# Kernel tuning notes

Hardware: AMD Instinct MI355X
Metric: run time of the kernel (lower is better)

## Reference

```python
import jax, jax.numpy as jnp
import numpy as np

D, H, KVH, HD = 2048, 16, 8, 128
D1, D2 = 32, 64  # get_decompose_dim(2048)
BITS = 8


def fake_quant(x, bits=BITS):
    # per-row (last-axis) symmetric fake quant with straight-through estimator
    qmax = float(2 ** (bits - 1) - 1)
    s = jnp.maximum(jnp.max(jnp.abs(x), axis=-1, keepdims=True) / qmax, 1e-8)
    q = jnp.clip(jnp.round(x / s), -qmax, qmax) * s
    return x + jax.lax.stop_gradient(q - x)


def rotate_half(x):
    h = x.shape[-1] // 2
    return jnp.concatenate([-x[..., h:], x[..., :h]], axis=-1)


def setup_inputs() -> dict:
    key = jax.random.key(0)
    ks = jax.random.split(key, 10)
    B, S = 1, 2048
    hidden_states = jax.random.normal(ks[0], (B, S, D), jnp.float32)
    # rotary embeddings
    inv_freq = 1.0 / (10000.0 ** (jnp.arange(0, HD, 2, dtype=jnp.float32) / HD))
    t = jnp.arange(S, dtype=jnp.float32)
    freqs = t[:, None] * inv_freq[None, :]
    emb = jnp.concatenate([freqs, freqs], axis=-1)
    cos, sin = jnp.cos(emb)[None], jnp.sin(emb)[None]  # [1,S,HD]
    # projection weights
    Wq = jax.random.normal(ks[1], (H * HD, D), jnp.float32) * 0.02
    Wk = jax.random.normal(ks[2], (KVH * HD, D), jnp.float32) * 0.02
    Wv = jax.random.normal(ks[3], (KVH * HD, D), jnp.float32) * 0.02
    Wo = jax.random.normal(ks[4], (D, H * HD), jnp.float32) * 0.02
    # learned invertible transforms (near-identity for conditioning)
    L = jnp.eye(D1) + 0.02 * jax.random.normal(ks[5], (D1, D1), jnp.float32)
    R = jnp.eye(D2) + 0.02 * jax.random.normal(ks[6], (D2, D2), jnp.float32)
    diag = 1.0 + 0.1 * jax.random.uniform(ks[7], (D,), jnp.float32)
    Tk = jnp.eye(HD) + 0.02 * jax.random.normal(ks[8], (HD, HD), jnp.float32)
    Tv = jnp.eye(HD) + 0.02 * jax.random.normal(ks[9], (HD, HD), jnp.float32)
    return dict(hidden_states=hidden_states, cos=cos, sin=sin, Wq=Wq, Wk=Wk,
                Wv=Wv, Wo=Wo, L=L, R=R, diag=diag, Tk=Tk, Tv=Tv)


def reference(hidden_states, cos, sin, Wq, Wk, Wv, Wo, L, R, diag, Tk, Tv):
    B, S, _ = hidden_states.shape
    groups = H // KVH
    scale = HD ** -0.5
    # ---- ln_trans: x' = (x * diag) @ kron(L, R) ----
    P = diag[:, None] * jnp.kron(L, R)               # [D, D]
    Pinv = jnp.kron(jnp.linalg.inv(L), jnp.linalg.inv(R)) * (1.0 / diag)[None, :]
    x = hidden_states @ P
    x_q = fake_quant(x)                               # per-token activation quant
    # ---- QKV with transform fused into weights (qa_trans), then weight quant ----
    q = x_q @ fake_quant(Wq @ Pinv.T).T               # [B,S,H*HD]
    k = x_q @ fake_quant(Wk @ Pinv.T).T               # [B,S,KVH*HD]
    Wv_eff = jnp.einsum('hd,khD->kdD', Tv, (Wv @ Pinv.T).reshape(KVH, HD, D))
    v = x_q @ fake_quant(Wv_eff.reshape(KVH * HD, D)).T  # v already in Tv space
    # ---- heads + RoPE ----
    q = q.reshape(B, S, H, HD).transpose(0, 2, 1, 3)
    k = k.reshape(B, S, KVH, HD).transpose(0, 2, 1, 3)
    v = v.reshape(B, S, KVH, HD).transpose(0, 2, 1, 3)
    c, s_ = cos[:, None], sin[:, None]                # [1,1,S,HD]
    q = q * c + rotate_half(q) * s_
    k = k * c + rotate_half(k) * s_
    # ---- kcache trans + quant: q @ inv(Tk)^T, k @ Tk (dot product preserved) ----
    q = q @ jnp.linalg.inv(Tk).T
    k = fake_quant(k @ Tk)
    v = fake_quant(v)
    # ---- eager causal attention with GQA ----
    k = jnp.repeat(k, groups, axis=1)
    v = jnp.repeat(v, groups, axis=1)
    scores = jnp.einsum('bhqd,bhkd->bhqk', q, k) * scale
    mask = jnp.tril(jnp.ones((S, S), bool))
    scores = jnp.where(mask, scores, jnp.finfo(scores.dtype).min)
    w = jax.nn.softmax(scores, axis=-1)
    o = jnp.einsum('bhqk,bhkd->bhqd', w, v)
    o = o.transpose(0, 2, 1, 3).reshape(B, S, H * HD)
    # ---- undo vcache trans per head, then quantized o_proj ----
    o = (o.reshape(B, S, H, HD) @ jnp.linalg.inv(Tv)).reshape(B, S, H * HD)
    out = fake_quant(o) @ fake_quant(Wo).T
    return out
```

## Files before the change

### kernel.cpp

```cpp
#include <hip/hip_runtime.h>
#include <math.h>

typedef unsigned short u16;
typedef __attribute__((ext_vector_type(8))) short bf16x8;
typedef __attribute__((ext_vector_type(4))) float f32x4;

__device__ __forceinline__ u16 f2bf(float x) {
    union { float f; unsigned int u; } c; c.f = x;
    unsigned int r = c.u + 0x7fffu + ((c.u >> 16) & 1u);
    return (u16)(r >> 16);
}
__device__ __forceinline__ float bf2f(u16 h) {
    union { unsigned int u; float f; } c; c.u = ((unsigned int)h) << 16;
    return c.f;
}
__device__ __forceinline__ bf16x8 ld16(const u16* p) {
    bf16x8 r;
    ((uint2*)&r)[0] = *(const uint2*)p;
    ((uint2*)&r)[1] = *(const uint2*)(p + 4);
    return r;
}
__device__ __forceinline__ void st8(u16* dst, uint4 r) {
    *(uint2*)dst = make_uint2(r.x, r.y);
    *(uint2*)(dst + 4) = make_uint2(r.z, r.w);
}

__global__ __launch_bounds__(1024) void gj4_kernel(
    const float* __restrict__ A0, float* __restrict__ I0,
    const float* __restrict__ A1, float* __restrict__ I1,
    const float* __restrict__ A2, float* __restrict__ I2,
    const float* __restrict__ A3, float* __restrict__ I3) {
    __shared__ float rowbuf[2][128];
    const float* A; float* out; int N;
    switch (blockIdx.x) {
        case 0:  A = A0; out = I0; N = 32;  break;
        case 1:  A = A1; out = I1; N = 64;  break;
        case 2:  A = A2; out = I2; N = 128; break;
        default: A = A3; out = I3; N = 128; break;
    }
    const int tid = threadIdx.x;
    const int i = tid >> 3, g = tid & 7, c0 = g * 16;
    const int rl = (i & 7) << 3;
    float r[16];
#pragma unroll
    for (int e = 0; e < 16; ++e) {
        int j = c0 + e;
        r[e] = (i < N && j < N) ? A[i * N + j] : ((i == j) ? 1.0f : 0.0f);
    }
    if (i == 0) {
        float ip = 1.0f / __shfl(r[0], rl, 64);
#pragma unroll
        for (int e = 0; e < 16; ++e)
            rowbuf[0][c0 + e] = (c0 + e == 0) ? ip : r[e] * ip;
    }
    __syncthreads();
    const int ng = N >> 4;
    for (int k16 = 0; k16 < ng; ++k16) {
#pragma unroll
        for (int e = 0; e < 16; ++e) {
            const int k = (k16 << 4) + e;
            const int pb = k & 1;
            float ci = __shfl(r[e], rl + k16, 64);
            float4 rb0 = *(const float4*)&rowbuf[pb][c0];
            float4 rb1 = *(const float4*)&rowbuf[pb][c0 + 4];
            float4 rb2 = *(const float4*)&rowbuf[pb][c0 + 8];
            float4 rb3 = *(const float4*)&rowbuf[pb][c0 + 12];
            float rb[16] = {rb0.x, rb0.y, rb0.z, rb0.w, rb1.x, rb1.y, rb1.z, rb1.w,
                            rb2.x, rb2.y, rb2.z, rb2.w, rb3.x, rb3.y, rb3.z, rb3.w};
            if (i == k) {
#pragma unroll
                for (int e2 = 0; e2 < 16; ++e2) r[e2] = rb[e2];
            } else {
#pragma unroll
                for (int e2 = 0; e2 < 16; ++e2) {
                    float v = (c0 + e2 == k) ? 0.0f : r[e2];
                    r[e2] = fmaf(-ci, rb[e2], v);
                }
            }
            if (k + 1 < N && i == k + 1) {
                const int en = (e + 1) & 15;
                const int gn = (e == 15) ? k16 + 1 : k16;
                float ip = 1.0f / __shfl(r[en], rl + gn, 64);
#pragma unroll
                for (int e2 = 0; e2 < 16; ++e2)
                    rowbuf[pb ^ 1][c0 + e2] = (c0 + e2 == k + 1) ? ip : r[e2] * ip;
            }
            __syncthreads();
        }
    }
    if (i < N)
#pragma unroll
        for (int e = 0; e < 16; ++e) {
            int j = c0 + e;
            if (j < N) out[i * N + j] = r[e];
        }
}

__global__ void rdiag_kernel(const float* __restrict__ d, float* __restrict__ rd) {
    int i = blockIdx.x * 256 + threadIdx.x;
    rd[i] = 1.0f / d[i];
}

template <int TA, int TB, int OUTQ>
__global__ __launch_bounds__(256) void kron_kernel(
    const float* __restrict__ X, const float* __restrict__ scIn,
    const float* __restrict__ A, const float* __restrict__ B,
    u16* __restrict__ Yq, float* __restrict__ Ysc, float* __restrict__ Yf) {
    __shared__ float Al[32 * 33];
    __shared__ float Bl[64 * 65];
    __shared__ float Xl[32 * 65];
    __shared__ float Tl[32 * 65];
    __shared__ float red[256];
    const int tid = threadIdx.x;
    for (int idx = tid; idx < 1024; idx += 256) {
        int c = idx >> 5, a = idx & 31;
        Al[c * 33 + a] = TA ? A[a * 32 + c] : A[c * 32 + a];
    }
    for (int idx = tid; idx < 4096; idx += 256) {
        int d = idx >> 6, b = idx & 63;
        Bl[d * 65 + b] = TB ? B[b * 64 + d] : B[d * 64 + b];
    }
    const int row = blockIdx.x;
    const float* xp = X + (size_t)row * 2048;
    for (int j = tid; j < 2048; j += 256)
        Xl[(j >> 6) * 65 + (j & 63)] = xp[j] * scIn[j];
    __syncthreads();

    const int c = tid >> 3, b0 = (tid & 7) * 8;
    float t[8];
#pragma unroll
    for (int jj = 0; jj < 8; ++jj) t[jj] = 0.0f;
    for (int d = 0; d < 64; ++d) {
        float xv = Xl[c * 65 + d];
#pragma unroll
        for (int jj = 0; jj < 8; ++jj)
            t[jj] = fmaf(xv, Bl[d * 65 + b0 + jj], t[jj]);
    }
#pragma unroll
    for (int jj = 0; jj < 8; ++jj) Tl[c * 65 + b0 + jj] = t[jj];
    __syncthreads();

    const int a = tid >> 3;
    float y[8];
#pragma unroll
    for (int jj = 0; jj < 8; ++jj) y[jj] = 0.0f;
    for (int c2 = 0; c2 < 32; ++c2) {
        float av = Al[c2 * 33 + a];
#pragma unroll
        for (int jj = 0; jj < 8; ++jj)
            y[jj] = fmaf(av, Tl[c2 * 65 + b0 + jj], y[jj]);
    }

    if (OUTQ) {
        float am = 0.0f;
#pragma unroll
        for (int jj = 0; jj < 8; ++jj) am = fmaxf(am, fabsf(y[jj]));
        red[tid] = am;
        __syncthreads();
        for (int s = 128; s > 0; s >>= 1) {
            if (tid < s) red[tid] = fmaxf(red[tid], red[tid + s]);
            __syncthreads();
        }
        float scale = fmaxf(red[0] / 127.0f, 1e-8f);
        if (tid == 0) Ysc[row] = scale;
        u16 qq[8];
#pragma unroll
        for (int e = 0; e < 8; ++e) {
            float v = rintf(y[e] / scale);
            v = fminf(fmaxf(v, -127.0f), 127.0f);
            qq[e] = f2bf(v);
        }
        uint4 pk;
        pk.x = qq[0] | ((unsigned)qq[1] << 16); pk.y = qq[2] | ((unsigned)qq[3] << 16);
        pk.z = qq[4] | ((unsigned)qq[5] << 16); pk.w = qq[6] | ((unsigned)qq[7] << 16);
        *(uint4*)(Yq + (size_t)row * 2048 + tid * 8) = pk;
    } else {
        float* yp = Yf + (size_t)row * 2048 + tid * 8;
        *(float4*)yp = make_float4(y[0], y[1], y[2], y[3]);
        *(float4*)(yp + 4) = make_float4(y[4], y[5], y[6], y[7]);
    }
}

__global__ void split_s_kernel(const float* __restrict__ in, int ld, int cols,
                               u16* __restrict__ hi, u16* __restrict__ lo) {
    int idx = (blockIdx.x * 256 + threadIdx.x) * 4;
    int r = idx / cols, c = idx % cols;
    float4 v = *(const float4*)(in + (size_t)r * ld + c);
    ushort4 h, l;
    h.x = f2bf(v.x); l.x = f2bf(v.x - bf2f(h.x));
    h.y = f2bf(v.y); l.y = f2bf(v.y - bf2f(h.y));
    h.z = f2bf(v.z); l.z = f2bf(v.z - bf2f(h.z));
    h.w = f2bf(v.w); l.w = f2bf(v.w - bf2f(h.w));
    *(ushort4*)(hi + idx) = h;
    *(ushort4*)(lo + idx) = l;
}

__global__ void split_t_kernel(const float* __restrict__ in, u16* __restrict__ hi,
                               u16* __restrict__ lo, int rows, int cols) {
    __shared__ float t[32][33];
    int bx = blockIdx.x, by = blockIdx.y;
    int lx = threadIdx.x & 31, ly = threadIdx.x >> 5;
    for (int r = ly; r < 32; r += 8)
        t[r][lx] = in[(size_t)(by * 32 + r) * cols + bx * 32 + lx];
    __syncthreads();
    for (int r = ly; r < 32; r += 8) {
        float v = t[lx][r];
        size_t o = (size_t)(bx * 32 + r) * rows + by * 32 + lx;
        u16 h = f2bf(v);
        hi[o] = h;
        lo[o] = f2bf(v - bf2f(h));
    }
}

__global__ void trans16_kernel(const u16* __restrict__ in, u16* __restrict__ out,
                               int rows, int cols) {
    __shared__ u16 t[64][72];
    int bx = blockIdx.x, by = blockIdx.y;
    int tid = threadIdx.x;
#pragma unroll
    for (int it = 0; it < 2; ++it) {
        int ii = tid + it * 256;
        int r = ii >> 3, c8 = (ii & 7) * 8;
        uint4 v = *(const uint4*)(in + (size_t)(by * 64 + r) * cols + bx * 64 + c8);
        st8(&t[r][c8], v);
    }
    __syncthreads();
#pragma unroll
    for (int it = 0; it < 2; ++it) {
        int ii = tid + it * 256;
        int r = ii >> 3, c8 = (ii & 7) * 8;
        u16 tmp[8];
#pragma unroll
        for (int e = 0; e < 8; ++e) tmp[e] = t[c8 + e][r];
        uint4 v;
        v.x = tmp[0] | ((unsigned)tmp[1] << 16); v.y = tmp[2] | ((unsigned)tmp[3] << 16);
        v.z = tmp[4] | ((unsigned)tmp[5] << 16); v.w = tmp[6] | ((unsigned)tmp[7] << 16);
        *(uint4*)(out + (size_t)(bx * 64 + r) * rows + by * 64 + c8) = v;
    }
}

__global__ __launch_bounds__(256) void gemm_kernel(
    const u16* __restrict__ Ah, const u16* __restrict__ Al, int lda, long aZ, int aDiv,
    const u16* __restrict__ Bh, const u16* __restrict__ Bl, int ldb, long bZ, int bDiv,
    float* __restrict__ C, int ldc, long cZ, int cDiv, int K, float alpha) {
    const int m0 = blockIdx.y * 128, n0 = blockIdx.x * 128;
    const int z = blockIdx.z;
    {
        long ao = (long)(z >> aDiv) * aZ;
        long bo = (long)(z >> bDiv) * bZ;
        Ah += ao; Al += ao; Bh += bo; Bl += bo;
    }
    __shared__ u16 Ash[2][2][128][36];
    __shared__ u16 Bsh[2][2][128][36];

    const int tid = threadIdx.x, lane = tid & 63, wave = tid >> 6;
    const int wr = wave >> 1, wc = wave & 1;
    const int fr = lane & 15, fg8 = (lane >> 4) * 8;
    const int srow = tid >> 2, cc8 = (tid & 3) * 8;

    f32x4 acc[4][4];
#pragma unroll
    for (int m = 0; m < 4; ++m)
#pragma unroll
        for (int n = 0; n < 4; ++n) acc[m][n] = (f32x4)0.0f;

    uint4 rah0, rah1, ral0, ral1, rbh0, rbh1, rbl0, rbl1;
    const size_t aoff0 = (size_t)(m0 + srow) * lda + cc8;
    const size_t aoff1 = aoff0 + (size_t)64 * lda;
    const size_t boff0 = (size_t)(n0 + srow) * ldb + cc8;
    const size_t boff1 = boff0 + (size_t)64 * ldb;

#define G_LOAD(k0) { \
    rah0 = *(const uint4*)(Ah + aoff0 + (k0)); rah1 = *(const uint4*)(Ah + aoff1 + (k0)); \
    ral0 = *(const uint4*)(Al + aoff0 + (k0)); ral1 = *(const uint4*)(Al + aoff1 + (k0)); \
    rbh0 = *(const uint4*)(Bh + boff0 + (k0)); rbh1 = *(const uint4*)(Bh + boff1 + (k0)); \
    rbl0 = *(const uint4*)(Bl + boff0 + (k0)); rbl1 = *(const uint4*)(Bl + boff1 + (k0)); }
#define G_STORE(b) { \
    st8(&Ash[b][0][srow][cc8], rah0); st8(&Ash[b][0][srow + 64][cc8], rah1); \
    st8(&Ash[b][1][srow][cc8], ral0); st8(&Ash[b][1][srow + 64][cc8], ral1); \
    st8(&Bsh[b][0][srow][cc8], rbh0); st8(&Bsh[b][0][srow + 64][cc8], rbh1); \
    st8(&Bsh[b][1][srow][cc8], rbl0); st8(&Bsh[b][1][srow + 64][cc8], rbl1); }

    const int nk = K >> 5;
    G_LOAD(0);
    G_STORE(0);
    __syncthreads();
    int cur = 0;
    for (int ik = 0; ik < nk; ++ik) {
        if (ik + 1 < nk) G_LOAD((ik + 1) << 5);
        bf16x8 bh[4], bl[4];
#pragma unroll
        for (int n = 0; n < 4; ++n) {
            bh[n] = ld16(&Bsh[cur][0][wc * 64 + n * 16 + fr][fg8]);
            bl[n] = ld16(&Bsh[cur][1][wc * 64 + n * 16 + fr][fg8]);
        }
#pragma unroll
        for (int m = 0; m < 4; ++m) {
            bf16x8 ah = ld16(&Ash[cur][0][wr * 64 + m * 16 + fr][fg8]);
            bf16x8 al = ld16(&Ash[cur][1][wr * 64 + m * 16 + fr][fg8]);
#pragma unroll
            for (int n = 0; n < 4; ++n) {
                acc[m][n] = __builtin_amdgcn_mfma_f32_16x16x32_bf16(ah, bh[n], acc[m][n], 0, 0, 0);
                acc[m][n] = __builtin_amdgcn_mfma_f32_16x16x32_bf16(ah, bl[n], acc[m][n], 0, 0, 0);
                acc[m][n] = __builtin_amdgcn_mfma_f32_16x16x32_bf16(al, bh[n], acc[m][n], 0, 0, 0);
            }
        }
        if (ik + 1 < nk) G_STORE(cur ^ 1);
        __syncthreads();
        cur ^= 1;
    }
    const long co = (long)(z >> cDiv) * cZ;
#pragma unroll
    for (int m = 0; m < 4; ++m) {
        int row_b = m0 + wr * 64 + m * 16 + (fg8 >> 1);
#pragma unroll
        for (int n = 0; n < 4; ++n) {
            int col = n0 + wc * 64 + n * 16 + fr;
#pragma unroll
            for (int j = 0; j < 4; ++j)
                C[co + (long)(row_b + j) * ldc + col] = alpha * acc[m][n][j];
        }
    }
#undef G_LOAD
#undef G_STORE
}

__global__ __launch_bounds__(256) void gemm_int_kernel(
    const u16* __restrict__ A, int lda, const float* __restrict__ sa,
    const u16* __restrict__ B, int ldb, const float* __restrict__ sb,
    float* __restrict__ C, int ldc, long aZ, long bZ, long cZ, int K) {
    const int m0 = blockIdx.y * 128, n0 = blockIdx.x * 128;
    const int z = blockIdx.z;
    A += (long)z * aZ; B += (long)z * bZ; C += (long)z * cZ;
    __shared__ u16 Ash[2][128][36];
    __shared__ u16 Bsh[2][128][36];
    const int tid = threadIdx.x, lane = tid & 63, wave = tid >> 6;
    const int wr = wave >> 1, wc = wave & 1;
    const int fr = lane & 15, fg8 = (lane >> 4) * 8;
    const int srow = tid >> 2, cc8 = (tid & 3) * 8;
    f32x4 acc[4][4];
#pragma unroll
    for (int m = 0; m < 4; ++m)
#pragma unroll
        for (int n = 0; n < 4; ++n) acc[m][n] = (f32x4)0.0f;

    uint4 ra0, ra1, rb0, rb1;
    const size_t aoff0 = (size_t)(m0 + srow) * lda + cc8;
    const size_t aoff1 = aoff0 + (size_t)64 * lda;
    const size_t boff0 = (size_t)(n0 + srow) * ldb + cc8;
    const size_t boff1 = boff0 + (size_t)64 * ldb;
#define GI_LOAD(k0) { \
    ra0 = *(const uint4*)(A + aoff0 + (k0)); ra1 = *(const uint4*)(A + aoff1 + (k0)); \
    rb0 = *(const uint4*)(B + boff0 + (k0)); rb1 = *(const uint4*)(B + boff1 + (k0)); }
#define GI_STORE(b) { \
    st8(&Ash[b][srow][cc8], ra0); st8(&Ash[b][srow + 64][cc8], ra1); \
    st8(&Bsh[b][srow][cc8], rb0); st8(&Bsh[b][srow + 64][cc8], rb1); }
    const int nk = K >> 5;
    GI_LOAD(0);
    GI_STORE(0);
    __syncthreads();
    int cur = 0;
    for (int ik = 0; ik < nk; ++ik) {
        if (ik + 1 < nk) GI_LOAD((ik + 1) << 5);
        bf16x8 bfr[4];
#pragma unroll
        for (int n = 0; n < 4; ++n)
            bfr[n] = ld16(&Bsh[cur][wc * 64 + n * 16 + fr][fg8]);
#pragma unroll
        for (int m = 0; m < 4; ++m) {
            bf16x8 ah = ld16(&Ash[cur][wr * 64 + m * 16 + fr][fg8]);
#pragma unroll
            for (int n = 0; n < 4; ++n)
                acc[m][n] = __builtin_amdgcn_mfma_f32_16x16x32_bf16(ah, bfr[n], acc[m][n], 0, 0, 0);
        }
        if (ik + 1 < nk) GI_STORE(cur ^ 1);
        __syncthreads();
        cur ^= 1;
    }
#pragma unroll
    for (int m = 0; m < 4; ++m) {
        int row_b = m0 + wr * 64 + m * 16 + (fg8 >> 1);
#pragma unroll
        for (int n = 0; n < 4; ++n) {
            int col = n0 + wc * 64 + n * 16 + fr;
            float sc = sb[col];
#pragma unroll
            for (int j = 0; j < 4; ++j)
                C[(long)(row_b + j) * ldc + col] = acc[m][n][j] * sa[row_b + j] * sc;
        }
    }
#undef GI_LOAD
#undef GI_STORE
}

__global__ void rowquant_int_kernel(const float* __restrict__ x, u16* __restrict__ qi,
                                    float* __restrict__ sc, int cols) {
    __shared__ float red[256];
    int row = blockIdx.x, tid = threadIdx.x;
    const float* p = x + (size_t)row * cols;
    u16* q = qi + (size_t)row * cols;
    float m = 0.0f;
    for (int j = tid; j < cols; j += 256) m = fmaxf(m, fabsf(p[j]));
    red[tid] = m; __syncthreads();
    for (int s = 128; s > 0; s >>= 1) {
        if (tid < s) red[tid] = fmaxf(red[tid], red[tid + s]);
        __syncthreads();
    }
    float scale = fmaxf(red[0] / 127.0f, 1e-8f);
    if (tid == 0) sc[row] = scale;
    for (int j = tid; j < cols; j += 256) {
        float v = rintf(p[j] / scale);
        v = fminf(fmaxf(v, -127.0f), 127.0f);
        q[j] = f2bf(v);
    }
}

__global__ void rowquant_v_kernel(const float* __restrict__ x, int ld, int cb,
                                  u16* __restrict__ qi, float* __restrict__ sc) {
    int row = blockIdx.x;
    int lane = threadIdx.x & 63, w = threadIdx.x >> 6;
    if (w > 0) return;
    const float* p = x + (size_t)(row >> 3) * ld + cb + (row & 7) * 128;
    u16* q = qi + (size_t)row * 128;
    float2 v = *(const float2*)(p + lane * 2);
    float m = fmaxf(fabsf(v.x), fabsf(v.y));
#pragma unroll
    for (int off = 1; off < 64; off <<= 1) m = fmaxf(m, __shfl_xor(m, off));
    float scale = fmaxf(m / 127.0f, 1e-8f);
    if (lane == 0) sc[row] = scale;
    float a = rintf(v.x / scale), b = rintf(v.y / scale);
    a = fminf(fmaxf(a, -127.0f), 127.0f);
    b = fminf(fmaxf(b, -127.0f), 127.0f);
    unsigned pk = f2bf(a) | ((unsigned)f2bf(b) << 16);
    *(unsigned*)(q + lane * 2) = pk;
}

__global__ void rope_kernel(float* __restrict__ x, int ld, int cb,
                            const float* __restrict__ c, const float* __restrict__ s,
                            int nh) {
    int idx = blockIdx.x * 256 + threadIdx.x;
    int d = idx & 63;
    int t = idx >> 6;
    int h = t % nh;
    int sq = t / nh;
    size_t base = (size_t)sq * ld + cb + h * 128;
    float a = x[base + d], b = x[base + d + 64];
    float c1 = c[sq * 128 + d], s1 = s[sq * 128 + d];
    float c2 = c[sq * 128 + d + 64], s2 = s[sq * 128 + d + 64];
    x[base + d] = a * c1 - b * s1;
    x[base + d + 64] = b * c2 + a * s2;
}

__global__ __launch_bounds__(256, 2) void flash_kernel(
    const float* __restrict__ q2f,
    const u16* __restrict__ k2i, const float* __restrict__ ksc,
    const u16* __restrict__ vTi, const float* __restrict__ vsc,
    float* __restrict__ obuf, float* __restrict__ mlbuf) {
    const int h = blockIdx.x, part = blockIdx.y, qt = 31 - blockIdx.z, g = h >> 1;
    __shared__ u16 Ksh[2][64 * 128];
    __shared__ u16 Vsh[2][128 * 64];
    __shared__ u16 Psh[4][16 * 64];
    __shared__ float Kss[2][64];
    __shared__ float Vss[2][64];

    const int tid = threadIdx.x, lane = tid & 63, w = tid >> 6;
    const int lc = lane & 15, lg = lane >> 4;
    const float scale = 0.08838834764831845f;
    const float LOG2E = 1.4426950408889634f;
    const float THR = 10.0f;

    bf16x8 qh[4], ql[4];
    {
        int s = qt * 64 + w * 16 + lc;
        const float* qp = q2f + (size_t)s * 2048 + h * 128 + lg * 8;
#pragma unroll
        for (int kk = 0; kk < 4; ++kk) {
            float4 v0 = *(const float4*)(qp + kk * 32);
            float4 v1 = *(const float4*)(qp + kk * 32 + 4);
            float vv[8] = {v0.x, v0.y, v0.z, v0.w, v1.x, v1.y, v1.z, v1.w};
#pragma unroll
            for (int e = 0; e < 8; ++e) {
                float x = vv[e] * scale;
                u16 hh = f2bf(x);
                qh[kk][e] = (short)hh;
                ql[kk][e] = (short)f2bf(x - bf2f(hh));
            }
        }
    }

    f32x4 acc_o[8];
#pragma unroll
    for (int nn = 0; nn < 8; ++nn) acc_o[nn] = (f32x4)0.0f;
    float mj = -1e30f, lj = 0.0f;

    const int p0cnt = (qt + 2) >> 1;
    const int tn = (part == 0) ? p0cnt : (qt + 1 - p0cnt);
    const int t0 = (part == 0) ? 0 : p0cnt;

    const int kr = tid >> 2, kc = tid & 3;
    const int vd = tid >> 1, vc0 = (tid & 1) * 4;
    uint4 kg0, kg1, kg2, kg3, vg0, vg1, vg2, vg3;
    float sreg = 0.0f;

#define STAGE_LOAD(tg) { \
    const int j0_ = (tg) * 64; \
    const u16* kp_ = k2i + (size_t)(j0_ + kr) * 1024 + g * 128; \
    kg0 = *(const uint4*)(kp_ + kc * 8); \
    kg1 = *(const uint4*)(kp_ + (kc + 4) * 8); \
    kg2 = *(const uint4*)(kp_ + (kc + 8) * 8); \
    kg3 = *(const uint4*)(kp_ + (kc + 12) * 8); \
    const u16* vp_ = vTi + (size_t)(g * 128 + vd) * 2048 + j0_; \
    vg0 = *(const uint4*)(vp_ + vc0 * 8); \
    vg1 = *(const uint4*)(vp_ + (vc0 + 1) * 8); \
    vg2 = *(const uint4*)(vp_ + (vc0 + 2) * 8); \
    vg3 = *(const uint4*)(vp_ + (vc0 + 3) * 8); \
    if (tid < 64) sreg = ksc[(j0_ + tid) * 8 + g] * LOG2E; \
    else if (tid < 128) sreg = vsc[(j0_ + tid - 64) * 8 + g]; }

#define STAGE_WRITE(b) { \
    *(uint4*)(&Ksh[b][kr * 128 + ((kc ^ (kr & 7)) << 3)]) = kg0; \
    *(uint4*)(&Ksh[b][kr * 128 + (((kc + 4) ^ (kr & 7)) << 3)]) = kg1; \
    *(uint4*)(&Ksh[b][kr * 128 + (((kc + 8) ^ (kr & 7)) << 3)]) = kg2; \
    *(uint4*)(&Ksh[b][kr * 128 + (((kc + 12) ^ (kr & 7)) << 3)]) = kg3; \
    *(uint4*)(&Vsh[b][vd * 64 + ((vc0 ^ (vd & 7)) << 3)]) = vg0; \
    *(uint4*)(&Vsh[b][vd * 64 + (((vc0 + 1) ^ (vd & 7)) << 3)]) = vg1; \
    *(uint4*)(&Vsh[b][vd * 64 + (((vc0 + 2) ^ (vd & 7)) << 3)]) = vg2; \
    *(uint4*)(&Vsh[b][vd * 64 + (((vc0 + 3) ^ (vd & 7)) << 3)]) = vg3; \
    if (tid < 64) Kss[b][tid] = sreg; \
    else if (tid < 128) Vss[b][tid - 64] = sreg; }

    if (tn > 0) {
        STAGE_LOAD(t0);
        STAGE_WRITE(0);
    }
    __syncthreads();
    for (int t = 0; t < tn; ++t) {
        const int cur = t & 1;
        const int tg = t0 + t;
        if (t + 1 < tn) STAGE_LOAD(t0 + t + 1);

        f32x4 accs[4];
#pragma unroll
        for (int n = 0; n < 4; ++n) accs[n] = (f32x4)0.0f;
#pragma unroll
        for (int n = 0; n < 4; ++n) {
#pragma unroll
            for (int kk = 0; kk < 4; ++kk) {
                bf16x8 kf = ld16(&Ksh[cur][(n * 16 + lc) * 128 + (((kk * 4 + lg) ^ (lc & 7)) << 3)]);
                accs[n] = __builtin_amdgcn_mfma_f32_16x16x32_bf16(kf, qh[kk], accs[n], 0, 0, 0);
                accs[n] = __builtin_amdgcn_mfma_f32_16x16x32_bf16(kf, ql[kk], accs[n], 0, 0, 0);
            }
        }
#pragma unroll
        for (int n = 0; n < 4; ++n)
#pragma unroll
            for (int j = 0; j < 4; ++j)
                accs[n][j] *= Kss[cur][n * 16 + lg * 4 + j];
        if (tg == qt) {
            int qg = qt * 64 + w * 16 + lc;
#pragma unroll
            for (int n = 0; n < 4; ++n)
#pragma unroll
                for (int j = 0; j < 4; ++j) {
                    int kgl = tg * 64 + n * 16 + lg * 4 + j;
                    if (kgl > qg) accs[n][j] = -3.0e38f;
                }
        }

        float pm = accs[0][0];
#pragma unroll
        for (int n = 0; n < 4; ++n)
#pragma unroll
            for (int j = 0; j < 4; ++j) pm = fmaxf(pm, accs[n][j]);
        pm = fmaxf(pm, __shfl_xor(pm, 16));
        pm = fmaxf(pm, __shfl_xor(pm, 32));
        bool need = pm > mj + THR;
        float mn = need ? pm : mj;
        float sf = need ? exp2f(mj - mn) : 1.0f;
        mj = mn;
        if (__any(need)) {
            float sfj[4];
#pragma unroll
            for (int j = 0; j < 4; ++j) sfj[j] = __shfl(sf, lg * 4 + j);
#pragma unroll
            for (int nn = 0; nn < 8; ++nn)
#pragma unroll
                for (int j = 0; j < 4; ++j) acc_o[nn][j] *= sfj[j];
        }
        float rowsum = 0.0f;
#pragma unroll
        for (int n = 0; n < 4; ++n)
#pragma unroll
            for (int j = 0; j < 4; ++j) {
                float p = exp2f(accs[n][j] - mj);
                accs[n][j] = p;
                rowsum += p;
            }
        rowsum += __shfl_xor(rowsum, 16);
        rowsum += __shfl_xor(rowsum, 32);
        lj = lj * sf + rowsum;

#pragma unroll
        for (int n = 0; n < 4; ++n)
#pragma unroll
            for (int jp = 0; jp < 2; ++jp) {
                int k = n * 16 + lg * 4 + jp * 2;
                unsigned val = f2bf(accs[n][jp * 2] * Vss[cur][k]) |
                               ((unsigned)f2bf(accs[n][jp * 2 + 1] * Vss[cur][k + 1]) << 16);
                int cch = k >> 3;
                *(unsigned*)(&Psh[w][lc * 64 + ((cch ^ (lc & 7)) << 3) + (k & 7)]) = val;
            }
        bf16x8 pf[2];
#pragma unroll
        for (int kk = 0; kk < 2; ++kk)
            pf[kk] = ld16(&Psh[w][lc * 64 + (((kk * 4 + lg) ^ (lc & 7)) << 3)]);

#pragma unroll
        for (int nn = 0; nn < 8; ++nn) {
            int d = nn * 16 + lc;
#pragma unroll
            for (int kk = 0; kk < 2; ++kk) {
                bf16x8 vf = ld16(&Vsh[cur][d * 64 + (((kk * 4 + lg) ^ (d & 7)) << 3)]);
                acc_o[nn] = __builtin_amdgcn_mfma_f32_16x16x32_bf16(pf[kk], vf, acc_o[nn], 0, 0, 0);
            }
        }
        if (t + 1 < tn) STAGE_WRITE(cur ^ 1);
        __syncthreads();
    }
#undef STAGE_LOAD
#undef STAGE_WRITE

    float* op = obuf + (size_t)part * 4194304 + ((size_t)h * 2048 + qt * 64 + w * 16) * 128;
#pragma unroll
    for (int nn = 0; nn < 8; ++nn)
#pragma unroll
        for (int j = 0; j < 4; ++j)
            op[(lg * 4 + j) * 128 + nn * 16 + lc] = acc_o[nn][j];
    if (lg == 0) {
        int rs = h * 2048 + qt * 64 + w * 16 + lc;
        mlbuf[part * 65536 + rs] = mj;
        mlbuf[part * 65536 + 32768 + rs] = lj;
    }
}

__global__ void combine_split_kernel(const float* __restrict__ o01,
                                     const float* __restrict__ ml,
                                     u16* __restrict__ oh, u16* __restrict__ ol) {
    int idx = blockIdx.x * 256 + threadIdx.x;
    int hs = idx >> 7;
    float m0 = ml[hs], l0 = ml[32768 + hs];
    float m1 = ml[65536 + hs], l1 = ml[98304 + hs];
    float m = fmaxf(m0, m1);
    float w0 = exp2f(m0 - m), w1 = exp2f(m1 - m);
    float l = l0 * w0 + l1 * w1;
    float v = (o01[idx] * w0 + o01[4194304 + idx] * w1) / l;
    u16 h = f2bf(v);
    oh[idx] = h;
    ol[idx] = f2bf(v - bf2f(h));
}

__global__ void add2_kernel(const float* __restrict__ a, const float* __restrict__ b,
                            float* __restrict__ o) {
    int i = (blockIdx.x * 256 + threadIdx.x) * 4;
    float4 x = *(const float4*)(a + i);
    float4 y = *(const float4*)(b + i);
    x.x += y.x; x.y += y.y; x.z += y.z; x.w += y.w;
    *(float4*)(o + i) = x;
}

extern "C" void kernel_launch(void* const* d_in, const int* in_sizes, int n_in,
                              void* d_out, int out_size, void* d_ws, size_t ws_size,
                              hipStream_t stream) {
    const float* hidden = (const float*)d_in[0];
    const float* cosp   = (const float*)d_in[1];
    const float* sinp   = (const float*)d_in[2];
    const float* Wq     = (const float*)d_in[3];
    const float* Wk     = (const float*)d_in[4];
    const float* Wv     = (const float*)d_in[5];
    const float* Wo     = (const float*)d_in[6];
    const float* Lp     = (const float*)d_in[7];
    const float* Rp     = (const float*)d_in[8];
    const float* diag   = (const float*)d_in[9];
    const float* Tkp    = (const float*)d_in[10];
    const float* Tvp    = (const float*)d_in[11];
    float* out = (float*)d_out;

    const size_t MiB = 1ull << 20;
    char* W = (char*)d_ws;
    auto F = [&](size_t mb) { return (float*)(W + mb * MiB); };
    auto U = [&](size_t mb) { return (u16*)(W + mb * MiB); };
    const long HP2 = 2097152;

    float* dsc   = (float*)d_out;
    float* invL  = dsc;
    float* invR  = dsc + 1024;
    float* invTk = dsc + 5120;
    float* invTv = dsc + 21504;
    u16* sm = (u16*)(dsc + 37888);
    u16* invTk_sh = sm;              u16* invTk_sl = sm + 16384;
    u16* TkT_sh   = sm + 2 * 16384;  u16* TkT_sl   = sm + 3 * 16384;
    u16* invTvT_sh= sm + 4 * 16384;  u16* invTvT_sl= sm + 5 * 16384;
    u16* TvT_sh   = sm + 6 * 16384;  u16* TvT_sl   = sm + 7 * 16384;

    auto gemm = [&](dim3 grid,
                    const u16* Ah, const u16* Al, int lda, long aZ, int aDiv,
                    const u16* Bh, const u16* Bl, int ldb, long bZ, int bDiv,
                    float* C, int ldc, long cZ, int cDiv, int K, float alpha) {
        gemm_kernel<<<grid, 256, 0, stream>>>(Ah, Al, lda, aZ, aDiv,
            Bh, Bl, ldb, bZ, bDiv, C, ldc, cZ, cDiv, K, alpha);
    };

    float* xs    = F(88);
    float* wqkvs = xs + 2048;
    float* wqs   = wqkvs;
    float* wks   = wqkvs + 2048;
    float* wvs   = wqkvs + 3072;
    float* k2s   = wqkvs + 4096;
    float* vs    = k2s + 16384;
    float* o2s   = vs + 16384;
    float* wos   = o2s + 2048;
    float* rdiag = wos + 2048;

    gj4_kernel<<<4, 1024, 0, stream>>>(Lp, invL, Rp, invR, Tkp, invTk, Tvp, invTv);
    rdiag_kernel<<<8, 256, 0, stream>>>(diag, rdiag);
    split_s_kernel<<<16, 256, 0, stream>>>(invTk, 128, 128, invTk_sh, invTk_sl);
    split_t_kernel<<<dim3(4, 4), 256, 0, stream>>>(Tkp, TkT_sh, TkT_sl, 128, 128);
    split_t_kernel<<<dim3(4, 4), 256, 0, stream>>>(invTv, invTvT_sh, invTvT_sl, 128, 128);
    split_t_kernel<<<dim3(4, 4), 256, 0, stream>>>(Tvp, TvT_sh, TvT_sl, 128, 128);

    u16* Xi    = U(0);
    u16* WQKVi = U(8);
    u16* WVi   = U(20);
    float* WvP = F(24);
    kron_kernel<0, 0, 1><<<2048, 256, 0, stream>>>(hidden, diag, Lp, Rp, Xi, xs, 0);
    kron_kernel<1, 1, 1><<<2048, 256, 0, stream>>>(Wq, rdiag, invL, invR, WQKVi, wqs, 0);
    kron_kernel<1, 1, 1><<<1024, 256, 0, stream>>>(Wk, rdiag, invL, invR, U(16), wks, 0);
    kron_kernel<1, 1, 0><<<1024, 256, 0, stream>>>(Wv, rdiag, invL, invR, 0, 0, WvP);

    u16* WVPt_s = U(32);
    split_t_kernel<<<dim3(64, 32), 256, 0, stream>>>(WvP, WVPt_s, WVPt_s + HP2, 1024, 2048);
    float* WVf = F(72);
    gemm(dim3(16, 1, 8), TvT_sh, TvT_sl, 128, 0, 0,
         WVPt_s, WVPt_s + HP2, 1024, 128, 0, WVf, 2048, (long)128 * 2048, 0, 128, 1.0f);
    rowquant_int_kernel<<<1024, 256, 0, stream>>>(WVf, WVi, wvs, 2048);

    float* QKVf = F(40);
    gemm_int_kernel<<<dim3(32, 16), 256, 0, stream>>>(Xi, 2048, xs, WQKVi, 2048, wqkvs,
                                                      QKVf, 4096, 0, 0, 0, 2048);

    rope_kernel<<<8192, 256, 0, stream>>>(QKVf, 4096, 0, cosp, sinp, 16);
    rope_kernel<<<4096, 256, 0, stream>>>(QKVf, 4096, 2048, cosp, sinp, 8);

    u16* KB_s = U(24);
    split_s_kernel<<<2048, 256, 0, stream>>>(QKVf + 2048, 4096, 1024, KB_s, KB_s + HP2);
    float* k2f = F(32);
    gemm(dim3(1, 16, 8), KB_s, KB_s + HP2, 1024, 128, 0,
         TkT_sh, TkT_sl, 128, 0, 0, k2f, 1024, 128, 0, 128, 1.0f);
    u16* k2i = U(8);
    rowquant_int_kernel<<<16384, 256, 0, stream>>>(k2f, k2i, k2s, 128);

    u16* Vi = U(12);
    rowquant_v_kernel<<<16384, 64, 0, stream>>>(QKVf, 4096, 3072, Vi, vs);
    u16* vTi = U(16);
    trans16_kernel<<<dim3(16, 32), 256, 0, stream>>>(Vi, vTi, 2048, 1024);

    u16* Q_s = U(24);
    split_s_kernel<<<4096, 256, 0, stream>>>(QKVf, 4096, 2048, Q_s, Q_s + 4194304);
    float* q2f = F(72);
    gemm(dim3(1, 16, 16), Q_s, Q_s + 4194304, 2048, 128, 0,
         invTk_sh, invTk_sl, 128, 0, 0, q2f, 2048, 128, 0, 128, 1.0f);

    float* o01 = F(40);
    float* ml  = F(32);
    flash_kernel<<<dim3(16, 2, 32), 256, 0, stream>>>(q2f, k2i, k2s, vTi, vs, o01, ml);
    u16* o_s = U(0);
    combine_split_kernel<<<16384, 256, 0, stream>>>(o01, ml, o_s, o_s + 4194304);

    float* o2f = F(16);
    gemm(dim3(1, 16, 16), o_s, o_s + 4194304, 128, 262144, 0,
         invTvT_sh, invTvT_sl, 128, 0, 0, o2f, 2048, 128, 0, 128, 1.0f);
    u16* o2i = U(32);
    rowquant_int_kernel<<<2048, 256, 0, stream>>>(o2f, o2i, o2s, 2048);
    u16* Woi = U(40);
    rowquant_int_kernel<<<2048, 256, 0, stream>>>(Wo, Woi, wos, 2048);
    float* C0 = F(48);
    gemm_int_kernel<<<dim3(16, 16, 2), 256, 0, stream>>>(o2i, 2048, o2s, Woi, 2048, wos,
                                                         C0, 2048, 1024, 1024, 4194304, 1024);
    add2_kernel<<<4096, 256, 0, stream>>>(C0, C0 + 4194304, out);

    (void)in_sizes; (void)n_in; (void)out_size; (void)ws_size;
}
```

Baseline: 511.0 us.

## Fuse fp32-to-bf16 split into GEMM loads and merge small prep kernels

```diff
diff --git a/kernel.cpp b/kernel.cpp
--- a/kernel.cpp
+++ b/kernel.cpp
@@ -23,6 +23,20 @@
 __device__ __forceinline__ void st8(u16* dst, uint4 r) {
     *(uint2*)dst = make_uint2(r.x, r.y);
     *(uint2*)(dst + 4) = make_uint2(r.z, r.w);
+}
+__device__ __forceinline__ void cvt8(const float4& v0, const float4& v1,
+                                     uint4& hi, uint4& lo) {
+    float vv[8] = {v0.x, v0.y, v0.z, v0.w, v1.x, v1.y, v1.z, v1.w};
+    u16 h[8], l[8];
+#pragma unroll
+    for (int e = 0; e < 8; ++e) {
+        h[e] = f2bf(vv[e]);
+        l[e] = f2bf(vv[e] - bf2f(h[e]));
+    }
+    hi.x = h[0] | ((unsigned)h[1] << 16); hi.y = h[2] | ((unsigned)h[3] << 16);
+    hi.z = h[4] | ((unsigned)h[5] << 16); hi.w = h[6] | ((unsigned)h[7] << 16);
+    lo.x = l[0] | ((unsigned)l[1] << 16); lo.y = l[2] | ((unsigned)l[3] << 16);
+    lo.z = l[4] | ((unsigned)l[5] << 16); lo.w = l[6] | ((unsigned)l[7] << 16);
 }
 
 __global__ __launch_bounds__(1024) void gj4_kernel(
@@ -96,12 +110,7 @@
         }
 }
 
-__global__ void rdiag_kernel(const float* __restrict__ d, float* __restrict__ rd) {
-    int i = blockIdx.x * 256 + threadIdx.x;
-    rd[i] = 1.0f / d[i];
-}
-
-template <int TA, int TB, int OUTQ>
+template <int TA, int TB, int OUTQ, int DIV>
 __global__ __launch_bounds__(256) void kron_kernel(
     const float* __restrict__ X, const float* __restrict__ scIn,
     const float* __restrict__ A, const float* __restrict__ B,
@@ -122,8 +131,10 @@
     }
     const int row = blockIdx.x;
     const float* xp = X + (size_t)row * 2048;
-    for (int j = tid; j < 2048; j += 256)
-        Xl[(j >> 6) * 65 + (j & 63)] = xp[j] * scIn[j];
+    for (int j = tid; j < 2048; j += 256) {
+        float sc = DIV ? (1.0f / scIn[j]) : scIn[j];
+        Xl[(j >> 6) * 65 + (j & 63)] = xp[j] * sc;
+    }
     __syncthreads();
 
     const int c = tid >> 3, b0 = (tid & 7) * 8;
@@ -212,30 +223,30 @@
     }
 }
 
-__global__ void trans16_kernel(const u16* __restrict__ in, u16* __restrict__ out,
-                               int rows, int cols) {
-    __shared__ u16 t[64][72];
+__global__ void split_t3_kernel(const float* __restrict__ i0, u16* __restrict__ h0,
+                                u16* __restrict__ l0,
+                                const float* __restrict__ i1, u16* __restrict__ h1,
+                                u16* __restrict__ l1,
+                                const float* __restrict__ i2, u16* __restrict__ h2,
+                                u16* __restrict__ l2) {
+    __shared__ float t[32][33];
+    const float* in; u16* hi; u16* lo;
+    switch (blockIdx.z) {
+        case 0:  in = i0; hi = h0; lo = l0; break;
+        case 1:  in = i1; hi = h1; lo = l1; break;
+        default: in = i2; hi = h2; lo = l2; break;
+    }
     int bx = blockIdx.x, by = blockIdx.y;
-    int tid = threadIdx.x;
-#pragma unroll
-    for (int it = 0; it < 2; ++it) {
-        int ii = tid + it * 256;
-        int r = ii >> 3, c8 = (ii & 7) * 8;
-        uint4 v = *(const uint4*)(in + (size_t)(by * 64 + r) * cols + bx * 64 + c8);
-        st8(&t[r][c8], v);
-    }
+    int lx = threadIdx.x & 31, ly = threadIdx.x >> 5;
+    for (int r = ly; r < 32; r += 8)
+        t[r][lx] = in[(size_t)(by * 32 + r) * 128 + bx * 32 + lx];
     __syncthreads();
-#pragma unroll
-    for (int it = 0; it < 2; ++it) {
-        int ii = tid + it * 256;
-        int r = ii >> 3, c8 = (ii & 7) * 8;
-        u16 tmp[8];
-#pragma unroll
-        for (int e = 0; e < 8; ++e) tmp[e] = t[c8 + e][r];
-        uint4 v;
-        v.x = tmp[0] | ((unsigned)tmp[1] << 16); v.y = tmp[2] | ((unsigned)tmp[3] << 16);
-        v.z = tmp[4] | ((unsigned)tmp[5] << 16); v.w = tmp[6] | ((unsigned)tmp[7] << 16);
-        *(uint4*)(out + (size_t)(bx * 64 + r) * rows + by * 64 + c8) = v;
+    for (int r = ly; r < 32; r += 8) {
+        float v = t[lx][r];
+        size_t o = (size_t)(bx * 32 + r) * 128 + by * 32 + lx;
+        u16 h = f2bf(v);
+        hi[o] = h;
+        lo[o] = f2bf(v - bf2f(h));
     }
 }
 
@@ -323,6 +334,95 @@
     }
 #undef G_LOAD
 #undef G_STORE
+}
+
+__global__ __launch_bounds__(256) void gemm_af32_kernel(
+    const float* __restrict__ A, int lda, long aZ, int aDiv,
+    const u16* __restrict__ Bh, const u16* __restrict__ Bl, int ldb, long bZ, int bDiv,
+    float* __restrict__ C, int ldc, long cZ, int cDiv, int K, float alpha) {
+    const int m0 = blockIdx.y * 128, n0 = blockIdx.x * 128;
+    const int z = blockIdx.z;
+    A += (long)(z >> aDiv) * aZ;
+    {
+        long bo = (long)(z >> bDiv) * bZ;
+        Bh += bo; Bl += bo;
+    }
+    __shared__ u16 Ash[2][2][128][36];
+    __shared__ u16 Bsh[2][2][128][36];
+
+    const int tid = threadIdx.x, lane = tid & 63, wave = tid >> 6;
+    const int wr = wave >> 1, wc = wave & 1;
+    const int fr = lane & 15, fg8 = (lane >> 4) * 8;
+    const int srow = tid >> 2, cc8 = (tid & 3) * 8;
+
+    f32x4 acc[4][4];
+#pragma unroll
+    for (int m = 0; m < 4; ++m)
+#pragma unroll
+        for (int n = 0; n < 4; ++n) acc[m][n] = (f32x4)0.0f;
+
+    float4 a00, a01, a10, a11;
+    uint4 rbh0, rbh1, rbl0, rbl1;
+    const size_t aoff0 = (size_t)(m0 + srow) * lda + cc8;
+    const size_t aoff1 = aoff0 + (size_t)64 * lda;
+    const size_t boff0 = (size_t)(n0 + srow) * ldb + cc8;
+    const size_t boff1 = boff0 + (size_t)64 * ldb;
+
+#define GA_LOAD(k0) { \
+    a00 = *(const float4*)(A + aoff0 + (k0)); a01 = *(const float4*)(A + aoff0 + (k0) + 4); \
+    a10 = *(const float4*)(A + aoff1 + (k0)); a11 = *(const float4*)(A + aoff1 + (k0) + 4); \
+    rbh0 = *(const uint4*)(Bh + boff0 + (k0)); rbh1 = *(const uint4*)(Bh + boff1 + (k0)); \
+    rbl0 = *(const uint4*)(Bl + boff0 + (k0)); rbl1 = *(const uint4*)(Bl + boff1 + (k0)); }
+#define GA_STORE(b) { \
+    uint4 h0_, l0_, h1_, l1_; \
+    cvt8(a00, a01, h0_, l0_); cvt8(a10, a11, h1_, l1_); \
+    st8(&Ash[b][0][srow][cc8], h0_); st8(&Ash[b][0][srow + 64][cc8], h1_); \
+    st8(&Ash[b][1][srow][cc8], l0_); st8(&Ash[b][1][srow + 64][cc8], l1_); \
+    st8(&Bsh[b][0][srow][cc8], rbh0); st8(&Bsh[b][0][srow + 64][cc8], rbh1); \
+    st8(&Bsh[b][1][srow][cc8], rbl0); st8(&Bsh[b][1][srow + 64][cc8], rbl1); }
+
+    const int nk = K >> 5;
+    GA_LOAD(0);
+    GA_STORE(0);
+    __syncthreads();
+    int cur = 0;
+    for (int ik = 0; ik < nk; ++ik) {
+        if (ik + 1 < nk) GA_LOAD((ik + 1) << 5);
+        bf16x8 bh[4], bl[4];
+#pragma unroll
+        for (int n = 0; n < 4; ++n) {
+            bh[n] = ld16(&Bsh[cur][0][wc * 64 + n * 16 + fr][fg8]);
+            bl[n] = ld16(&Bsh[cur][1][wc * 64 + n * 16 + fr][fg8]);
+        }
+#pragma unroll
+        for (int m = 0; m < 4; ++m) {
+            bf16x8 ah = ld16(&Ash[cur][0][wr * 64 + m * 16 + fr][fg8]);
+            bf16x8 al = ld16(&Ash[cur][1][wr * 64 + m * 16 + fr][fg8]);
+#pragma unroll
+            for (int n = 0; n < 4; ++n) {
+                acc[m][n] = __builtin_amdgcn_mfma_f32_16x16x32_bf16(ah, bh[n], acc[m][n], 0, 0, 0);
+                acc[m][n] = __builtin_amdgcn_mfma_f32_16x16x32_bf16(ah, bl[n], acc[m][n], 0, 0, 0);
+                acc[m][n] = __builtin_amdgcn_mfma_f32_16x16x32_bf16(al, bh[n], acc[m][n], 0, 0, 0);
+            }
+        }
+        if (ik + 1 < nk) GA_STORE(cur ^ 1);
+        __syncthreads();
+        cur ^= 1;
+    }
+    const long co = (long)(z >> cDiv) * cZ;
+#pragma unroll
+    for (int m = 0; m < 4; ++m) {
+        int row_b = m0 + wr * 64 + m * 16 + (fg8 >> 1);
+#pragma unroll
+        for (int n = 0; n < 4; ++n) {
+            int col = n0 + wc * 64 + n * 16 + fr;
+#pragma unroll
+            for (int j = 0; j < 4; ++j)
+                C[co + (long)(row_b + j) * ldc + col] = alpha * acc[m][n][j];
+        }
+    }
+#undef GA_LOAD
+#undef GA_STORE
 }
 
 __global__ __launch_bounds__(256) void gemm_int_kernel(
@@ -415,13 +515,11 @@
     }
 }
 
-__global__ void rowquant_v_kernel(const float* __restrict__ x, int ld, int cb,
-                                  u16* __restrict__ qi, float* __restrict__ sc) {
-    int row = blockIdx.x;
-    int lane = threadIdx.x & 63, w = threadIdx.x >> 6;
-    if (w > 0) return;
-    const float* p = x + (size_t)(row >> 3) * ld + cb + (row & 7) * 128;
-    u16* q = qi + (size_t)row * 128;
+__global__ void rowquant_w_kernel(const float* __restrict__ x, u16* __restrict__ qi,
+                                  float* __restrict__ sc) {
+    int row = blockIdx.x * 4 + (threadIdx.x >> 6);
+    int lane = threadIdx.x & 63;
+    const float* p = x + (size_t)row * 128;
     float2 v = *(const float2*)(p + lane * 2);
     float m = fmaxf(fabsf(v.x), fabsf(v.y));
 #pragma unroll
@@ -432,7 +530,52 @@
     a = fminf(fmaxf(a, -127.0f), 127.0f);
     b = fminf(fmaxf(b, -127.0f), 127.0f);
     unsigned pk = f2bf(a) | ((unsigned)f2bf(b) << 16);
-    *(unsigned*)(q + lane * 2) = pk;
+    *(unsigned*)(qi + (size_t)row * 128 + lane * 2) = pk;
+}
+
+__global__ __launch_bounds__(256) void quantT_v_kernel(
+    const float* __restrict__ QKVf, u16* __restrict__ vTi, float* __restrict__ vs) {
+    __shared__ u16 tile[128][72];
+    const int st = blockIdx.x, g = blockIdx.y;
+    const int t = threadIdx.x;
+    const int sl = t >> 2, dc = (t & 3) * 32;
+    const int s = st * 64 + sl;
+    const float* p = QKVf + (size_t)s * 4096 + 3072 + g * 128 + dc;
+    float4 vr[8];
+    float m = 0.0f;
+#pragma unroll
+    for (int q = 0; q < 8; ++q) {
+        vr[q] = *(const float4*)(p + q * 4);
+        m = fmaxf(m, fmaxf(fmaxf(fabsf(vr[q].x), fabsf(vr[q].y)),
+                           fmaxf(fabsf(vr[q].z), fabsf(vr[q].w))));
+    }
+    m = fmaxf(m, __shfl_xor(m, 1));
+    m = fmaxf(m, __shfl_xor(m, 2));
+    float scale = fmaxf(m / 127.0f, 1e-8f);
+    if ((t & 3) == 0) vs[s * 8 + g] = scale;
+#pragma unroll
+    for (int q = 0; q < 8; ++q) {
+        float vv[4] = {vr[q].x, vr[q].y, vr[q].z, vr[q].w};
+#pragma unroll
+        for (int e = 0; e < 4; ++e) {
+            float qv = rintf(vv[e] / scale);
+            qv = fminf(fmaxf(qv, -127.0f), 127.0f);
+            tile[dc + q * 4 + e][sl] = f2bf(qv);
+        }
+    }
+    __syncthreads();
+    const int d = t >> 1, sc0 = (t & 1) * 32;
+    u16* dst = vTi + (size_t)(g * 128 + d) * 2048 + st * 64 + sc0;
+#pragma unroll
+    for (int q = 0; q < 4; ++q) {
+        u16 tmp[8];
+#pragma unroll
+        for (int e = 0; e < 8; ++e) tmp[e] = tile[d][sc0 + q * 8 + e];
+        uint4 v;
+        v.x = tmp[0] | ((unsigned)tmp[1] << 16); v.y = tmp[2] | ((unsigned)tmp[3] << 16);
+        v.z = tmp[4] | ((unsigned)tmp[5] << 16); v.w = tmp[6] | ((unsigned)tmp[7] << 16);
+        *(uint4*)(dst + q * 8) = v;
+    }
 }
 
 __global__ void rope_kernel(float* __restrict__ x, int ld, int cb,
@@ -643,9 +786,9 @@
     }
 }
 
-__global__ void combine_split_kernel(const float* __restrict__ o01,
-                                     const float* __restrict__ ml,
-                                     u16* __restrict__ oh, u16* __restrict__ ol) {
+__global__ void combine_kernel(const float* __restrict__ o01,
+                               const float* __restrict__ ml,
+                               float* __restrict__ of) {
     int idx = blockIdx.x * 256 + threadIdx.x;
     int hs = idx >> 7;
     float m0 = ml[hs], l0 = ml[32768 + hs];
@@ -653,10 +796,7 @@
     float m = fmaxf(m0, m1);
     float w0 = exp2f(m0 - m), w1 = exp2f(m1 - m);
     float l = l0 * w0 + l1 * w1;
-    float v = (o01[idx] * w0 + o01[4194304 + idx] * w1) / l;
-    u16 h = f2bf(v);
-    oh[idx] = h;
-    ol[idx] = f2bf(v - bf2f(h));
+    of[idx] = (o01[idx] * w0 + o01[4194304 + idx] * w1) / l;
 }
 
 __global__ void add2_kernel(const float* __restrict__ a, const float* __restrict__ b,
@@ -702,14 +842,6 @@
     u16* invTvT_sh= sm + 4 * 16384;  u16* invTvT_sl= sm + 5 * 16384;
     u16* TvT_sh   = sm + 6 * 16384;  u16* TvT_sl   = sm + 7 * 16384;
 
-    auto gemm = [&](dim3 grid,
-                    const u16* Ah, const u16* Al, int lda, long aZ, int aDiv,
-                    const u16* Bh, const u16* Bl, int ldb, long bZ, int bDiv,
-                    float* C, int ldc, long cZ, int cDiv, int K, float alpha) {
-        gemm_kernel<<<grid, 256, 0, stream>>>(Ah, Al, lda, aZ, aDiv,
-            Bh, Bl, ldb, bZ, bDiv, C, ldc, cZ, cDiv, K, alpha);
-    };
-
     float* xs    = F(88);
     float* wqkvs = xs + 2048;
     float* wqs   = wqkvs;
@@ -719,29 +851,27 @@
     float* vs    = k2s + 16384;
     float* o2s   = vs + 16384;
     float* wos   = o2s + 2048;
-    float* rdiag = wos + 2048;
 
     gj4_kernel<<<4, 1024, 0, stream>>>(Lp, invL, Rp, invR, Tkp, invTk, Tvp, invTv);
-    rdiag_kernel<<<8, 256, 0, stream>>>(diag, rdiag);
     split_s_kernel<<<16, 256, 0, stream>>>(invTk, 128, 128, invTk_sh, invTk_sl);
-    split_t_kernel<<<dim3(4, 4), 256, 0, stream>>>(Tkp, TkT_sh, TkT_sl, 128, 128);
-    split_t_kernel<<<dim3(4, 4), 256, 0, stream>>>(invTv, invTvT_sh, invTvT_sl, 128, 128);
-    split_t_kernel<<<dim3(4, 4), 256, 0, stream>>>(Tvp, TvT_sh, TvT_sl, 128, 128);
+    split_t3_kernel<<<dim3(4, 4, 3), 256, 0, stream>>>(
+        Tkp, TkT_sh, TkT_sl, invTv, invTvT_sh, invTvT_sl, Tvp, TvT_sh, TvT_sl);
 
     u16* Xi    = U(0);
     u16* WQKVi = U(8);
     u16* WVi   = U(20);
     float* WvP = F(24);
-    kron_kernel<0, 0, 1><<<2048, 256, 0, stream>>>(hidden, diag, Lp, Rp, Xi, xs, 0);
-    kron_kernel<1, 1, 1><<<2048, 256, 0, stream>>>(Wq, rdiag, invL, invR, WQKVi, wqs, 0);
-    kron_kernel<1, 1, 1><<<1024, 256, 0, stream>>>(Wk, rdiag, invL, invR, U(16), wks, 0);
-    kron_kernel<1, 1, 0><<<1024, 256, 0, stream>>>(Wv, rdiag, invL, invR, 0, 0, WvP);
+    kron_kernel<0, 0, 1, 0><<<2048, 256, 0, stream>>>(hidden, diag, Lp, Rp, Xi, xs, 0);
+    kron_kernel<1, 1, 1, 1><<<2048, 256, 0, stream>>>(Wq, diag, invL, invR, WQKVi, wqs, 0);
+    kron_kernel<1, 1, 1, 1><<<1024, 256, 0, stream>>>(Wk, diag, invL, invR, U(16), wks, 0);
+    kron_kernel<1, 1, 0, 1><<<1024, 256, 0, stream>>>(Wv, diag, invL, invR, 0, 0, WvP);
 
     u16* WVPt_s = U(32);
     split_t_kernel<<<dim3(64, 32), 256, 0, stream>>>(WvP, WVPt_s, WVPt_s + HP2, 1024, 2048);
     float* WVf = F(72);
-    gemm(dim3(16, 1, 8), TvT_sh, TvT_sl, 128, 0, 0,
-         WVPt_s, WVPt_s + HP2, 1024, 128, 0, WVf, 2048, (long)128 * 2048, 0, 128, 1.0f);
+    gemm_kernel<<<dim3(16, 1, 8), 256, 0, stream>>>(
+        TvT_sh, TvT_sl, 128, 0, 0, WVPt_s, WVPt_s + HP2, 1024, 128, 0,
+        WVf, 2048, (long)128 * 2048, 0, 128, 1.0f);
     rowquant_int_kernel<<<1024, 256, 0, stream>>>(WVf, WVi, wvs, 2048);
 
     float* QKVf = F(40);
@@ -751,34 +881,31 @@
     rope_kernel<<<8192, 256, 0, stream>>>(QKVf, 4096, 0, cosp, sinp, 16);
     rope_kernel<<<4096, 256, 0, stream>>>(QKVf, 4096, 2048, cosp, sinp, 8);
 
-    u16* KB_s = U(24);
-    split_s_kernel<<<2048, 256, 0, stream>>>(QKVf + 2048, 4096, 1024, KB_s, KB_s + HP2);
     float* k2f = F(32);
-    gemm(dim3(1, 16, 8), KB_s, KB_s + HP2, 1024, 128, 0,
-         TkT_sh, TkT_sl, 128, 0, 0, k2f, 1024, 128, 0, 128, 1.0f);
+    gemm_af32_kernel<<<dim3(1, 16, 8), 256, 0, stream>>>(
+        QKVf + 2048, 4096, 128, 0, TkT_sh, TkT_sl, 128, 0, 0,
+        k2f, 1024, 128, 0, 128, 1.0f);
     u16* k2i = U(8);
-    rowquant_int_kernel<<<16384, 256, 0, stream>>>(k2f, k2i, k2s, 128);
-
-    u16* Vi = U(12);
-    rowquant_v_kernel<<<16384, 64, 0, stream>>>(QKVf, 4096, 3072, Vi, vs);
+    rowquant_w_kernel<<<4096, 256, 0, stream>>>(k2f, k2i, k2s);
+
     u16* vTi = U(16);
-    trans16_kernel<<<dim3(16, 32), 256, 0, stream>>>(Vi, vTi, 2048, 1024);
-
-    u16* Q_s = U(24);
-    split_s_kernel<<<4096, 256, 0, stream>>>(QKVf, 4096, 2048, Q_s, Q_s + 4194304);
+    quantT_v_kernel<<<dim3(32, 8), 256, 0, stream>>>(QKVf, vTi, vs);
+
     float* q2f = F(72);
-    gemm(dim3(1, 16, 16), Q_s, Q_s + 4194304, 2048, 128, 0,
-         invTk_sh, invTk_sl, 128, 0, 0, q2f, 2048, 128, 0, 128, 1.0f);
+    gemm_af32_kernel<<<dim3(1, 16, 16), 256, 0, stream>>>(
+        QKVf, 4096, 128, 0, invTk_sh, invTk_sl, 128, 0, 0,
+        q2f, 2048, 128, 0, 128, 1.0f);
 
     float* o01 = F(40);
     float* ml  = F(32);
     flash_kernel<<<dim3(16, 2, 32), 256, 0, stream>>>(q2f, k2i, k2s, vTi, vs, o01, ml);
-    u16* o_s = U(0);
-    combine_split_kernel<<<16384, 256, 0, stream>>>(o01, ml, o_s, o_s + 4194304);
+    float* of = F(0);
+    combine_kernel<<<16384, 256, 0, stream>>>(o01, ml, of);
 
     float* o2f = F(16);
-    gemm(dim3(1, 16, 16), o_s, o_s + 4194304, 128, 262144, 0,
-         invTvT_sh, invTvT_sl, 128, 0, 0, o2f, 2048, 128, 0, 128, 1.0f);
+    gemm_af32_kernel<<<dim3(1, 16, 16), 256, 0, stream>>>(
+        of, 128, 262144, 0, invTvT_sh, invTvT_sl, 128, 0, 0,
+        o2f, 2048, 128, 0, 128, 1.0f);
     u16* o2i = U(32);
     rowquant_int_kernel<<<2048, 256, 0, stream>>>(o2f, o2i, o2s, 2048);
     u16* Woi = U(40);
```

Result: faster. 497.7 us (-2.6%).
